# Optimization experiments

Measured on AMD Instinct MI355X. Metric: run time of the kernel, lower is better.

The kernel has to match this reference:

```python
import jax, jax.numpy as jnp
import numpy as np

B, S, D, H = 2, 2048, 1024, 16
DH = D // H

def setup_inputs() -> dict:
    key = jax.random.key(0)
    ks = jax.random.split(key, 9)
    s = 1.0 / np.sqrt(D)
    def lin(k):
        kw, kb = jax.random.split(k)
        W = jax.random.uniform(kw, (D, D), jnp.float32, -s, s)
        b = jax.random.uniform(kb, (D,), jnp.float32, -s, s)
        return W, b
    Wq, bq = lin(ks[0]); Wk, bk = lin(ks[1]); Wv, bv = lin(ks[2]); Wo, bo = lin(ks[3])
    x = jax.random.normal(ks[4], (B, S, D), jnp.float32)
    return {"x": x, "Wq": Wq, "bq": bq, "Wk": Wk, "bk": bk,
            "Wv": Wv, "bv": bv, "Wo": Wo, "bo": bo}

def _split_heads(t):
    # [B,S,D] -> [B,H,S,DH]
    return t.reshape(B, S, H, DH).transpose(0, 2, 1, 3)

def reference(x, Wq, bq, Wk, bk, Wv, bv, Wo, bo):
    # torch Linear: y = x @ W.T + b
    q = _split_heads(x @ Wq.T + bq)
    k = _split_heads(x @ Wk.T + bk)
    v = _split_heads(x @ Wv.T + bv)
    scores = jnp.einsum('bhqd,bhkd->bhqk', q, k) / jnp.sqrt(jnp.float32(DH))
    p = jax.nn.softmax(scores, axis=-1)  # dropout is identity in eval
    o = jnp.einsum('bhqk,bhkd->bhqd', p, v)
    o = o.transpose(0, 2, 1, 3).reshape(B, S, D)  # combine heads
    return o @ Wo.T + bo
```

## Files before the change

### kernel.cpp

```cpp
#include <hip/hip_runtime.h>


typedef __bf16 bf16;
typedef bf16 bf16x8 __attribute__((ext_vector_type(8)));
typedef bf16 bf16x4 __attribute__((ext_vector_type(4)));
typedef short s16x4 __attribute__((ext_vector_type(4)));
typedef float f32x4 __attribute__((ext_vector_type(4)));

#define MFMA32(a, b, c) __builtin_amdgcn_mfma_f32_16x16x32_bf16(a, b, c, 0, 0, 0)

#if __has_builtin(__builtin_amdgcn_mfma_f32_16x16x16bf16_1k)
#define HAVE_MFMA16 1
#define MFMA16(a, b, c) __builtin_amdgcn_mfma_f32_16x16x16bf16_1k(a, b, c, 0, 0, 0)
#else
#define HAVE_MFMA16 0
#endif

union pk4 { bf16x4 h; s16x4 s; unsigned int d[2]; };

__global__ __launch_bounds__(256)
void cvt_bf16(const float* __restrict__ x,  const float* __restrict__ Wq,
              const float* __restrict__ Wk, const float* __restrict__ Wv,
              const float* __restrict__ Wo,
              bf16* __restrict__ xb, bf16* __restrict__ wqb, bf16* __restrict__ wkb,
              bf16* __restrict__ wvb, bf16* __restrict__ wob)
{
    const int idx = blockIdx.x * 256 + threadIdx.x;
    const float* src; bf16* dst; int off;
    if (idx < 1048576) { src = x; dst = xb; off = idx; }
    else {
        const int r = idx - 1048576;
        const int seg = r >> 18;
        off = r & 262143;
        src = (seg == 0) ? Wq : (seg == 1) ? Wk : (seg == 2) ? Wv : Wo;
        dst = (seg == 0) ? wqb : (seg == 1) ? wkb : (seg == 2) ? wvb : wob;
    }
    const float4 v = ((const float4*)src)[off];
    bf16x4 o = {(bf16)v.x, (bf16)v.y, (bf16)v.z, (bf16)v.w};
    *(bf16x4*)(dst + (size_t)off * 4) = o;
}

__global__ __launch_bounds__(256)
void qkv_gemm(const bf16* __restrict__ xb,
              const bf16* __restrict__ wqb, const float* __restrict__ bq,
              const bf16* __restrict__ wkb, const float* __restrict__ bk,
              const bf16* __restrict__ wvb, const float* __restrict__ bv,
              bf16* __restrict__ q_ws, bf16* __restrict__ k_ws, bf16* __restrict__ v_ws)
{
    const int z = blockIdx.z;
    const bf16*  W    = (z == 0) ? wqb : (z == 1) ? wkb : wvb;
    const float* bias = (z == 0) ? bq  : (z == 1) ? bk  : bv;

    __shared__ bf16 As[128][40];
    __shared__ bf16 Bs[128][40];
    __shared__ bf16 Vt[64][132];

    const int m0 = blockIdx.x * 128;
    const int n0 = blockIdx.y * 128;
    const int t    = threadIdx.x;
    const int wave = t >> 6;
    const int lane = t & 63;
    const int lr   = lane & 15;
    const int quad = lane >> 4;
    const int wm = (wave & 1) * 64;
    const int wn = (wave >> 1) * 64;

    f32x4 acc[4][4] = {};

    for (int k0 = 0; k0 < 1024; k0 += 32) {
        #pragma unroll
        for (int u = 0; u < 2; u++) {
            const int c = t + u * 256;
            const int row = c >> 2, coloff = (c & 3) * 8;
            *(bf16x8*)&As[row][coloff] =
                *(const bf16x8*)(xb + (size_t)(m0 + row) * 1024 + k0 + coloff);
            *(bf16x8*)&Bs[row][coloff] =
                *(const bf16x8*)(W + (size_t)(n0 + row) * 1024 + k0 + coloff);
        }
        __syncthreads();

        bf16x8 af[4], bfr[4];
        #pragma unroll
        for (int i = 0; i < 4; i++) af[i]  = *(const bf16x8*)&As[wm + i*16 + lr][quad*8];
        #pragma unroll
        for (int j = 0; j < 4; j++) bfr[j] = *(const bf16x8*)&Bs[wn + j*16 + lr][quad*8];
        #pragma unroll
        for (int i = 0; i < 4; i++)
            #pragma unroll
            for (int j = 0; j < 4; j++)
                acc[i][j] = MFMA32(af[i], bfr[j], acc[i][j]);
        __syncthreads();
    }

    if (z < 2) {
        bf16* dstb = (z == 0) ? q_ws : k_ws;
        const float sc = (z == 0) ? 0.125f : 1.0f;
        #pragma unroll
        for (int j = 0; j < 4; j++) {
            const int col = n0 + wn + j * 16 + lr;
            const float bb = bias[col];
            const int h  = col >> 6;
            const int dh = col & 63;
            #pragma unroll
            for (int i = 0; i < 4; i++)
                #pragma unroll
                for (int r = 0; r < 4; r++) {
                    const int row = m0 + wm + i * 16 + quad * 4 + r;
                    const int bi = row >> 11, si = row & 2047;
                    dstb[(((size_t)bi * 16 + h) * 2048 + si) * 64 + dh] =
                        (bf16)((acc[i][j][r] + bb) * sc);
                }
        }
    } else {
        const int bi = m0 >> 11, si0 = m0 & 2047;
        #pragma unroll
        for (int ph = 0; ph < 2; ph++) {
            if ((wave >> 1) == ph) {
                #pragma unroll
                for (int j = 0; j < 4; j++) {
                    const float bb = bias[n0 + ph * 64 + j * 16 + lr];
                    #pragma unroll
                    for (int i = 0; i < 4; i++)
                        #pragma unroll
                        for (int r = 0; r < 4; r++)
                            Vt[j * 16 + lr][wm + i * 16 + quad * 4 + r] =
                                (bf16)(acc[i][j][r] + bb);
                }
            }
            __syncthreads();
            const int c  = t >> 2;
            const int sc_ = (t & 3) * 32;
            const int col = n0 + ph * 64 + c;
            const int h = col >> 6, dh = col & 63;
            bf16* dst = v_ws + (((size_t)bi * 16 + h) * 64 + dh) * 2048 + si0 + sc_;
            #pragma unroll
            for (int e = 0; e < 4; e++)
                *(bf16x8*)(dst + e * 8) = *(const bf16x8*)&Vt[c][sc_ + e * 8];
            __syncthreads();
        }
    }
}

__global__ __launch_bounds__(256, 4)
void attn(const bf16* __restrict__ q_ws, const bf16* __restrict__ k_ws,
          const bf16* __restrict__ v_ws, bf16* __restrict__ o_ws)
{
    const int qt = blockIdx.x;
    const int bh = blockIdx.y;
    const int b_ = bh >> 4, h = bh & 15;

    const bf16* qbase = q_ws + (size_t)bh * 2048 * 64;
    const bf16* kbase = k_ws + (size_t)bh * 2048 * 64;
    const bf16* vbase = v_ws + (size_t)bh * 64 * 2048;

    __shared__ bf16 Ks[128][72];
    __shared__ bf16 Vs[64][136];

    const int t    = threadIdx.x;
    const int wave = t >> 6;
    const int lane = t & 63;
    const int lr   = lane & 15;
    const int quad = lane >> 4;

    bf16x8 aq[2];
    #pragma unroll
    for (int kc = 0; kc < 2; kc++)
        aq[kc] = *(const bf16x8*)(qbase +
            (size_t)(qt*64 + wave*16 + lr) * 64 + kc*32 + quad*8);

    float m_i = -1e30f, l_i = 0.f;
    f32x4 o_acc[4] = {};
    const float C = 1.44269504f;

    for (int kt = 0; kt < 16; kt++) {
        __syncthreads();
        #pragma unroll
        for (int u = 0; u < 4; u++) {
            const int c = t + u * 256;
            *(bf16x8*)&Ks[c >> 3][(c & 7) * 8] =
                *(const bf16x8*)(kbase + (size_t)kt * 128 * 64 + c * 8);
            const int d = c >> 4, off = (c & 15) * 8;
            *(bf16x8*)&Vs[d][off] =
                *(const bf16x8*)(vbase + (size_t)d * 2048 + kt*128 + off);
        }
        __syncthreads();

        f32x4 sacc[8];
        #pragma unroll
        for (int j = 0; j < 8; j++) {
            bf16x8 kf0 = *(const bf16x8*)&Ks[j*16 + lr][quad*8];
            bf16x8 kf1 = *(const bf16x8*)&Ks[j*16 + lr][32 + quad*8];
            f32x4 a = {0.f, 0.f, 0.f, 0.f};
            a = MFMA32(kf0, aq[0], a);
            a = MFMA32(kf1, aq[1], a);
            sacc[j] = a;
        }

        float m = -1e30f;
        #pragma unroll
        for (int j = 0; j < 8; j++)
            #pragma unroll
            for (int r = 0; r < 4; r++) m = fmaxf(m, sacc[j][r]);
        m = fmaxf(m, __shfl_xor(m, 16));
        m = fmaxf(m, __shfl_xor(m, 32));
        const float nm = fmaxf(m_i, m);
        const float al = exp2f((m_i - nm) * C);
        m_i = nm;
        const float nmc = nm * C;
        float rs = 0.f;
        #pragma unroll
        for (int j = 0; j < 8; j++)
            #pragma unroll
            for (int r = 0; r < 4; r++) {
                const float p = exp2f(fmaf(sacc[j][r], C, -nmc));
                sacc[j][r] = p;
                rs += p;
            }
        rs += __shfl_xor(rs, 16);
        rs += __shfl_xor(rs, 32);
        l_i = l_i * al + rs;

        float alr[4];
        #pragma unroll
        for (int r = 0; r < 4; r++) alr[r] = __shfl(al, quad * 4 + r);
        #pragma unroll
        for (int n = 0; n < 4; n++)
            #pragma unroll
            for (int r = 0; r < 4; r++) o_acc[n][r] *= alr[r];

#if HAVE_MFMA16
        #pragma unroll
        for (int j = 0; j < 8; j++) {
            pk4 pf;
            pf.h = bf16x4{(bf16)sacc[j][0], (bf16)sacc[j][1],
                          (bf16)sacc[j][2], (bf16)sacc[j][3]};
            #pragma unroll
            for (int n = 0; n < 4; n++) {
                pk4 bf_;
                *(unsigned long long*)bf_.d =
                    *(const unsigned long long*)&Vs[n*16 + lr][j*16 + quad*4];
                o_acc[n] = MFMA16(pf.s, bf_.s, o_acc[n]);
            }
        }
#else
        unsigned int u0[8], u1[8];
        #pragma unroll
        for (int j = 0; j < 8; j++) {
            pk4 pf;
            pf.h = bf16x4{(bf16)sacc[j][0], (bf16)sacc[j][1],
                          (bf16)sacc[j][2], (bf16)sacc[j][3]};
            u0[j] = pf.d[0]; u1[j] = pf.d[1];
        }
        const int src0 = 32 * (quad & 1) + lr;
        const int src1 = src0 + 16;
        #pragma unroll
        for (int c = 0; c < 4; c++) {
            unsigned int w0a = __shfl(u0[2*c], src0),   w0b = __shfl(u0[2*c+1], src0);
            unsigned int w1a = __shfl(u1[2*c], src0),   w1b = __shfl(u1[2*c+1], src0);
            unsigned int w2a = __shfl(u0[2*c], src1),   w2b = __shfl(u0[2*c+1], src1);
            unsigned int w3a = __shfl(u1[2*c], src1),   w3b = __shfl(u1[2*c+1], src1);
            unsigned int fr[4];
            fr[0] = (quad >= 2) ? w0b : w0a;
            fr[1] = (quad >= 2) ? w1b : w1a;
            fr[2] = (quad >= 2) ? w2b : w2a;
            fr[3] = (quad >= 2) ? w3b : w3a;
            bf16x8 pf8 = *(bf16x8*)fr;
            #pragma unroll
            for (int n = 0; n < 4; n++) {
                bf16x8 bv8 = *(const bf16x8*)&Vs[n*16 + lr][c*32 + quad*8];
                o_acc[n] = MFMA32(pf8, bv8, o_acc[n]);
            }
        }
#endif
    }

    float lv[4];
    #pragma unroll
    for (int r = 0; r < 4; r++) lv[r] = __shfl(l_i, quad * 4 + r);
    #pragma unroll
    for (int n = 0; n < 4; n++)
        #pragma unroll
        for (int r = 0; r < 4; r++) {
            const int s   = qt*64 + wave*16 + quad*4 + r;
            const int col = h*64 + n*16 + lr;
            o_ws[((size_t)b_ * 2048 + s) * 1024 + col] = (bf16)(o_acc[n][r] / lv[r]);
        }
}

__global__ __launch_bounds__(256)
void out_gemm(const bf16* __restrict__ o_ws,
              const bf16* __restrict__ wob, const float* __restrict__ bo,
              float* __restrict__ out)
{
    __shared__ bf16 As[128][40];
    __shared__ bf16 Bs[128][40];

    const int m0 = blockIdx.x * 128;
    const int n0 = blockIdx.y * 128;
    const int t    = threadIdx.x;
    const int wave = t >> 6;
    const int lane = t & 63;
    const int lr   = lane & 15;
    const int quad = lane >> 4;
    const int wm = (wave & 1) * 64;
    const int wn = (wave >> 1) * 64;

    f32x4 acc[4][4] = {};

    for (int k0 = 0; k0 < 1024; k0 += 32) {
        #pragma unroll
        for (int u = 0; u < 2; u++) {
            const int c = t + u * 256;
            const int row = c >> 2, coloff = (c & 3) * 8;
            *(bf16x8*)&As[row][coloff] =
                *(const bf16x8*)(o_ws + (size_t)(m0 + row) * 1024 + k0 + coloff);
            *(bf16x8*)&Bs[row][coloff] =
                *(const bf16x8*)(wob + (size_t)(n0 + row) * 1024 + k0 + coloff);
        }
        __syncthreads();

        bf16x8 af[4], bfr[4];
        #pragma unroll
        for (int i = 0; i < 4; i++) af[i]  = *(const bf16x8*)&As[wm + i*16 + lr][quad*8];
        #pragma unroll
        for (int j = 0; j < 4; j++) bfr[j] = *(const bf16x8*)&Bs[wn + j*16 + lr][quad*8];
        #pragma unroll
        for (int i = 0; i < 4; i++)
            #pragma unroll
            for (int j = 0; j < 4; j++)
                acc[i][j] = MFMA32(af[i], bfr[j], acc[i][j]);
        __syncthreads();
    }

    #pragma unroll
    for (int j = 0; j < 4; j++) {
        const int col = n0 + wn + j * 16 + lr;
        const float bb = bo[col];
        #pragma unroll
        for (int i = 0; i < 4; i++)
            #pragma unroll
            for (int r = 0; r < 4; r++) {
                const int row = m0 + wm + i * 16 + quad * 4 + r;
                out[(size_t)row * 1024 + col] = acc[i][j][r] + bb;
            }
    }
}

extern "C" void kernel_launch(void* const* d_in, const int* in_sizes, int n_in,
                              void* d_out, int out_size, void* d_ws, size_t ws_size,
                              hipStream_t stream) {
    (void)in_sizes; (void)n_in; (void)out_size; (void)ws_size;
    const float* x  = (const float*)d_in[0];
    const float* Wq = (const float*)d_in[1];
    const float* bq = (const float*)d_in[2];
    const float* Wk = (const float*)d_in[3];
    const float* bk = (const float*)d_in[4];
    const float* Wv = (const float*)d_in[5];
    const float* bv = (const float*)d_in[6];
    const float* Wo = (const float*)d_in[7];
    const float* bo = (const float*)d_in[8];
    float* out = (float*)d_out;

    char* ws = (char*)d_ws;
    const size_t MB = 1024 * 1024;
    bf16* xb   = (bf16*)(ws);
    bf16* wqb  = (bf16*)(ws + 8 * MB);
    bf16* wkb  = (bf16*)(ws + 10 * MB);
    bf16* wvb  = (bf16*)(ws + 12 * MB);
    bf16* wob  = (bf16*)(ws + 14 * MB);
    bf16* q_ws = (bf16*)(ws + 16 * MB);
    bf16* k_ws = (bf16*)(ws + 24 * MB);
    bf16* v_ws = (bf16*)(ws + 32 * MB);
    bf16* o_ws = (bf16*)(ws + 40 * MB);

    hipLaunchKernelGGL(cvt_bf16, dim3(8192), dim3(256), 0, stream,
                       x, Wq, Wk, Wv, Wo, xb, wqb, wkb, wvb, wob);
    hipLaunchKernelGGL(qkv_gemm, dim3(32, 8, 3), dim3(256), 0, stream,
                       xb, wqb, bq, wkb, bk, wvb, bv, q_ws, k_ws, v_ws);
    hipLaunchKernelGGL(attn, dim3(32, 32), dim3(256), 0, stream,
                       q_ws, k_ws, v_ws, o_ws);
    hipLaunchKernelGGL(out_gemm, dim3(32, 8), dim3(256), 0, stream,
                       o_ws, wob, bo, out);
}
```

Baseline: 251.5 us.

## Use direct global-to-LDS loads in GEMMs and transpose attention PV accumulator

The QKV and output GEMMs now stage their A/B tiles with global_load_lds (direct global-to-shared DMA) instead of loading through registers and storing to shared memory, and drop the LDS row padding so the rows are contiguous as that instruction requires. The attention PV product swaps the MFMA operands so each lane holds its own query row, which removes the per-iteration shuffles of the rescale factor and the final normalizer and allows vectorized 8-byte stores of the output. The unpadded LDS layout may add bank conflicts on fragment reads, and the GEMMs still have no multi-buffering to hide load latency.

Result: faster. 243.8 us (-3.1%).

```diff
diff --git a/kernel.cpp b/kernel.cpp
--- a/kernel.cpp
+++ b/kernel.cpp
@@ -15,6 +15,10 @@
 #else
 #define HAVE_MFMA16 0
 #endif
+
+#define GLL(g, l) __builtin_amdgcn_global_load_lds(                              \
+    (const __attribute__((address_space(1))) void*)(const void*)(g),             \
+    (__attribute__((address_space(3))) void*)(void*)(l), 16, 0, 0)
 
 union pk4 { bf16x4 h; s16x4 s; unsigned int d[2]; };
 
@@ -51,8 +55,8 @@
     const bf16*  W    = (z == 0) ? wqb : (z == 1) ? wkb : wvb;
     const float* bias = (z == 0) ? bq  : (z == 1) ? bk  : bv;
 
-    __shared__ bf16 As[128][40];
-    __shared__ bf16 Bs[128][40];
+    __shared__ bf16 As[128][32];
+    __shared__ bf16 Bs[128][32];
     __shared__ bf16 Vt[64][132];
 
     const int m0 = blockIdx.x * 128;
@@ -65,18 +69,24 @@
     const int wm = (wave & 1) * 64;
     const int wn = (wave >> 1) * 64;
 
+    const int srow = wave * 32 + (lane >> 2);
+    const int scol = (lane & 3) * 8;
+    const bf16* ga0 = xb + (size_t)(m0 + srow) * 1024 + scol;
+    const bf16* ga1 = xb + (size_t)(m0 + srow + 16) * 1024 + scol;
+    const bf16* gb0 = W  + (size_t)(n0 + srow) * 1024 + scol;
+    const bf16* gb1 = W  + (size_t)(n0 + srow + 16) * 1024 + scol;
+    bf16* la0 = &As[srow][scol];
+    bf16* la1 = &As[srow + 16][scol];
+    bf16* lb0 = &Bs[srow][scol];
+    bf16* lb1 = &Bs[srow + 16][scol];
+
     f32x4 acc[4][4] = {};
 
     for (int k0 = 0; k0 < 1024; k0 += 32) {
-        #pragma unroll
-        for (int u = 0; u < 2; u++) {
-            const int c = t + u * 256;
-            const int row = c >> 2, coloff = (c & 3) * 8;
-            *(bf16x8*)&As[row][coloff] =
-                *(const bf16x8*)(xb + (size_t)(m0 + row) * 1024 + k0 + coloff);
-            *(bf16x8*)&Bs[row][coloff] =
-                *(const bf16x8*)(W + (size_t)(n0 + row) * 1024 + k0 + coloff);
-        }
+        GLL(ga0 + k0, la0);
+        GLL(ga1 + k0, la1);
+        GLL(gb0 + k0, lb0);
+        GLL(gb1 + k0, lb1);
         __syncthreads();
 
         bf16x8 af[4], bfr[4];
@@ -169,7 +179,7 @@
             (size_t)(qt*64 + wave*16 + lr) * 64 + kc*32 + quad*8);
 
     float m_i = -1e30f, l_i = 0.f;
-    f32x4 o_acc[4] = {};
+    f32x4 o_accT[4] = {};
     const float C = 1.44269504f;
 
     for (int kt = 0; kt < 16; kt++) {
@@ -216,17 +226,13 @@
                 sacc[j][r] = p;
                 rs += p;
             }
+        #pragma unroll
+        for (int n = 0; n < 4; n++)
+            #pragma unroll
+            for (int r = 0; r < 4; r++) o_accT[n][r] *= al;
         rs += __shfl_xor(rs, 16);
         rs += __shfl_xor(rs, 32);
         l_i = l_i * al + rs;
-
-        float alr[4];
-        #pragma unroll
-        for (int r = 0; r < 4; r++) alr[r] = __shfl(al, quad * 4 + r);
-        #pragma unroll
-        for (int n = 0; n < 4; n++)
-            #pragma unroll
-            for (int r = 0; r < 4; r++) o_acc[n][r] *= alr[r];
 
 #if HAVE_MFMA16
         #pragma unroll
@@ -235,56 +241,54 @@
             pf.h = bf16x4{(bf16)sacc[j][0], (bf16)sacc[j][1],
                           (bf16)sacc[j][2], (bf16)sacc[j][3]};
             #pragma unroll
-            for (int n = 0; n < 4; n++) {
-                pk4 bf_;
-                *(unsigned long long*)bf_.d =
-                    *(const unsigned long long*)&Vs[n*16 + lr][j*16 + quad*4];
-                o_acc[n] = MFMA16(pf.s, bf_.s, o_acc[n]);
+            for (int fb = 0; fb < 4; fb++) {
+                pk4 vf;
+                *(unsigned long long*)vf.d =
+                    *(const unsigned long long*)&Vs[fb*16 + lr][j*16 + quad*4];
+                o_accT[fb] = MFMA16(vf.s, pf.s, o_accT[fb]);
             }
         }
 #else
-        unsigned int u0[8], u1[8];
+        unsigned int p0[8], p1[8];
         #pragma unroll
         for (int j = 0; j < 8; j++) {
             pk4 pf;
             pf.h = bf16x4{(bf16)sacc[j][0], (bf16)sacc[j][1],
                           (bf16)sacc[j][2], (bf16)sacc[j][3]};
-            u0[j] = pf.d[0]; u1[j] = pf.d[1];
-        }
-        const int src0 = 32 * (quad & 1) + lr;
-        const int src1 = src0 + 16;
+            p0[j] = pf.d[0]; p1[j] = pf.d[1];
+        }
+        const int srcA = lr + 16 * ((2 * quad) & 3);
+        const int srcB = lr + 16 * ((2 * quad + 1) & 3);
+        const bool hi = (quad >> 1) != 0;
         #pragma unroll
         for (int c = 0; c < 4; c++) {
-            unsigned int w0a = __shfl(u0[2*c], src0),   w0b = __shfl(u0[2*c+1], src0);
-            unsigned int w1a = __shfl(u1[2*c], src0),   w1b = __shfl(u1[2*c+1], src0);
-            unsigned int w2a = __shfl(u0[2*c], src1),   w2b = __shfl(u0[2*c+1], src1);
-            unsigned int w3a = __shfl(u1[2*c], src1),   w3b = __shfl(u1[2*c+1], src1);
+            unsigned int a0 = __shfl(p0[2*c], srcA), a1 = __shfl(p0[2*c+1], srcA);
+            unsigned int b0 = __shfl(p1[2*c], srcA), b1 = __shfl(p1[2*c+1], srcA);
+            unsigned int c0 = __shfl(p0[2*c], srcB), c1 = __shfl(p0[2*c+1], srcB);
+            unsigned int d0 = __shfl(p1[2*c], srcB), d1 = __shfl(p1[2*c+1], srcB);
             unsigned int fr[4];
-            fr[0] = (quad >= 2) ? w0b : w0a;
-            fr[1] = (quad >= 2) ? w1b : w1a;
-            fr[2] = (quad >= 2) ? w2b : w2a;
-            fr[3] = (quad >= 2) ? w3b : w3a;
+            fr[0] = hi ? a1 : a0;
+            fr[1] = hi ? b1 : b0;
+            fr[2] = hi ? c1 : c0;
+            fr[3] = hi ? d1 : d0;
             bf16x8 pf8 = *(bf16x8*)fr;
             #pragma unroll
-            for (int n = 0; n < 4; n++) {
-                bf16x8 bv8 = *(const bf16x8*)&Vs[n*16 + lr][c*32 + quad*8];
-                o_acc[n] = MFMA32(pf8, bv8, o_acc[n]);
+            for (int fb = 0; fb < 4; fb++) {
+                bf16x8 vf8 = *(const bf16x8*)&Vs[fb*16 + lr][c*32 + quad*8];
+                o_accT[fb] = MFMA32(vf8, pf8, o_accT[fb]);
             }
         }
 #endif
     }
 
-    float lv[4];
+    const float inv = 1.0f / l_i;
+    const int s = qt*64 + wave*16 + lr;
     #pragma unroll
-    for (int r = 0; r < 4; r++) lv[r] = __shfl(l_i, quad * 4 + r);
-    #pragma unroll
-    for (int n = 0; n < 4; n++)
-        #pragma unroll
-        for (int r = 0; r < 4; r++) {
-            const int s   = qt*64 + wave*16 + quad*4 + r;
-            const int col = h*64 + n*16 + lr;
-            o_ws[((size_t)b_ * 2048 + s) * 1024 + col] = (bf16)(o_acc[n][r] / lv[r]);
-        }
+    for (int fb = 0; fb < 4; fb++) {
+        bf16x4 ov = {(bf16)(o_accT[fb][0] * inv), (bf16)(o_accT[fb][1] * inv),
+                     (bf16)(o_accT[fb][2] * inv), (bf16)(o_accT[fb][3] * inv)};
+        *(bf16x4*)(o_ws + ((size_t)b_ * 2048 + s) * 1024 + h*64 + fb*16 + quad*4) = ov;
+    }
 }
 
 __global__ __launch_bounds__(256)
@@ -292,8 +296,8 @@
               const bf16* __restrict__ wob, const float* __restrict__ bo,
               float* __restrict__ out)
 {
-    __shared__ bf16 As[128][40];
-    __shared__ bf16 Bs[128][40];
+    __shared__ bf16 As[128][32];
+    __shared__ bf16 Bs[128][32];
 
     const int m0 = blockIdx.x * 128;
     const int n0 = blockIdx.y * 128;
@@ -305,18 +309,24 @@
     const int wm = (wave & 1) * 64;
     const int wn = (wave >> 1) * 64;
 
+    const int srow = wave * 32 + (lane >> 2);
+    const int scol = (lane & 3) * 8;
+    const bf16* ga0 = o_ws + (size_t)(m0 + srow) * 1024 + scol;
+    const bf16* ga1 = o_ws + (size_t)(m0 + srow + 16) * 1024 + scol;
+    const bf16* gb0 = wob  + (size_t)(n0 + srow) * 1024 + scol;
+    const bf16* gb1 = wob  + (size_t)(n0 + srow + 16) * 1024 + scol;
+    bf16* la0 = &As[srow][scol];
+    bf16* la1 = &As[srow + 16][scol];
+    bf16* lb0 = &Bs[srow][scol];
+    bf16* lb1 = &Bs[srow + 16][scol];
+
     f32x4 acc[4][4] = {};
 
     for (int k0 = 0; k0 < 1024; k0 += 32) {
-        #pragma unroll
-        for (int u = 0; u < 2; u++) {
-            const int c = t + u * 256;
-            const int row = c >> 2, coloff = (c & 3) * 8;
-            *(bf16x8*)&As[row][coloff] =
-                *(const bf16x8*)(o_ws + (size_t)(m0 + row) * 1024 + k0 + coloff);
-            *(bf16x8*)&Bs[row][coloff] =
-                *(const bf16x8*)(wob + (size_t)(n0 + row) * 1024 + k0 + coloff);
-        }
+        GLL(ga0 + k0, la0);
+        GLL(ga1 + k0, la1);
+        GLL(gb0 + k0, lb0);
+        GLL(gb1 + k0, lb1);
         __syncthreads();
 
         bf16x8 af[4], bfr[4];
```
